# Performance work log

Hardware: AMD Instinct MI355X
Metric: run time of the kernel (lower is better)

Reference implementation:

```python
import jax, jax.numpy as jnp
import numpy as np
from jax import lax

B, N, C = 8, 8192, 64
ODR, K, OUT = 4, 32, 128
S = N // ODR
EPS = 1e-5


def _lbr(h, W, b, g, be):
    # h: [M, K, Cin] -> linear -> BN (training-mode batch stats over (M,K) per channel) -> relu
    y = jnp.einsum('mki,oi->mko', h, W) + b
    mean = y.mean(axis=(0, 1))
    var = ((y - mean) ** 2).mean(axis=(0, 1))  # biased var, as torch BN uses for normalization
    y = (y - mean) * lax.rsqrt(var + EPS) * g + be
    return jax.nn.relu(y)


def setup_inputs() -> dict:
    key = jax.random.key(0)
    ks = jax.random.split(key, 12)
    x = jax.random.normal(ks[0], (B, N, C), dtype=jnp.float32)
    coor = jax.random.normal(ks[1], (B, N, 3), dtype=jnp.float32)
    indx = jax.random.permutation(ks[2], N)[:S]  # like torch.randperm(N)[:S]
    w1 = jax.random.normal(ks[3], (OUT, 2 * C), dtype=jnp.float32) * (2 * C) ** -0.5
    b1 = jax.random.normal(ks[4], (OUT,), dtype=jnp.float32) * 0.01
    g1 = jax.random.uniform(ks[5], (OUT,), dtype=jnp.float32, minval=0.5, maxval=1.5)
    be1 = jax.random.normal(ks[6], (OUT,), dtype=jnp.float32) * 0.01
    w2 = jax.random.normal(ks[7], (OUT, OUT), dtype=jnp.float32) * OUT ** -0.5
    b2 = jax.random.normal(ks[8], (OUT,), dtype=jnp.float32) * 0.01
    g2 = jax.random.uniform(ks[9], (OUT,), dtype=jnp.float32, minval=0.5, maxval=1.5)
    be2 = jax.random.normal(ks[10], (OUT,), dtype=jnp.float32) * 0.01
    return dict(x=x, coor=coor, indx=indx, w1=w1, b1=b1, g1=g1, be1=be1,
                w2=w2, b2=b2, g2=g2, be2=be2)


def reference(x, coor, indx, w1, b1, g1, be1, w2, b2, g2, be2):
    sampled_coor = coor[:, indx, :]  # [B,S,3]
    sampled_x = x[:, indx, :]        # [B,S,C]
    # pairwise squared distances [B,S,N]
    dist = jnp.sum((coor[:, None, :, :] - sampled_coor[:, :, None, :]) ** 2, axis=-1)
    # k smallest distances == argsort(dist)[..., :K]
    _, knn_idx = lax.top_k(-dist, K)  # [B,S,K]
    knn_x = jax.vmap(lambda xb, ib: xb[ib])(x, knn_idx)  # [B,S,K,C]
    rep_x = jnp.broadcast_to(sampled_x[:, :, None, :], (x.shape[0], S, K, x.shape[2]))
    feat = jnp.concatenate([rep_x, knn_x - rep_x], axis=-1)  # [B,S,K,2C]
    feat = feat.reshape(x.shape[0] * S, K, 2 * x.shape[2])
    h = _lbr(feat, w1, b1, g1, be1)
    h = _lbr(h, w2, b2, g2, be2)
    h = h.reshape(x.shape[0], S, K, -1)
    out = jnp.max(h, axis=2)  # [B,S,OUT]
    return out, sampled_coor
```

## Files before the change

### kernel.cpp

```cpp
#include <hip/hip_runtime.h>
#include <stdint.h>


#define N_    8192
#define GPB_  16

typedef __attribute__((ext_vector_type(8))) short bf8;
typedef __attribute__((ext_vector_type(16))) float f32x16;
typedef __attribute__((ext_vector_type(2))) float f32x2;

__device__ __forceinline__ unsigned int bf1u(float f) {
  unsigned int u = __float_as_uint(f);
  return (u + 0x7fffu + ((u >> 16) & 1u)) >> 16;
}
__device__ __forceinline__ unsigned int bfpair(float lo, float hi) {
  return bf1u(lo) | (bf1u(hi) << 16);
}

__device__ __forceinline__ f32x2 pk_add(f32x2 a, f32x2 b) {
  f32x2 d;
  asm("v_pk_add_f32 %0, %1, %2" : "=v"(d) : "v"(a), "v"(b));
  return d;
}
__device__ __forceinline__ f32x2 pk_mul(f32x2 a, f32x2 b) {
  f32x2 d;
  asm("v_pk_mul_f32 %0, %1, %2" : "=v"(d) : "v"(a), "v"(b));
  return d;
}

__global__ __launch_bounds__(256) void kprep(const float* __restrict__ w1,
                                             const float* __restrict__ w2,
                                             const float* __restrict__ coor,
                                             const int* __restrict__ indx,
                                             unsigned short* __restrict__ w1b,
                                             unsigned short* __restrict__ w2b,
                                             float* __restrict__ outc,
                                             float* __restrict__ soa) {
  int e = blockIdx.x * 256 + threadIdx.x;
  if (e < 16384) {
    w1b[e] = (unsigned short)bf1u(w1[e]);
  } else if (e < 32768) {
    int e2 = e - 16384;
    w2b[e2] = (unsigned short)bf1u(w2[e2]);
  } else if (e < 81920) {
    int e2 = e - 32768;
    int bs = e2 / 3, c = e2 - bs * 3;
    int b = bs >> 11, s = bs & 2047;
    outc[e2] = coor[(b * N_ + indx[s]) * 3 + c];
  } else {
    int p = e - 81920;
    const int b = p >> 13, i = p & 8191;
    const float* src = coor + (size_t)p * 3;
    float* dst = soa + b * 24576;
    dst[i]         = src[0];
    dst[8192 + i]  = src[1];
    dst[16384 + i] = src[2];
  }
}

__global__ __launch_bounds__(256, 8) void kknn(const float* __restrict__ soa,
                                               const int* __restrict__ indx,
                                               int* __restrict__ knn) {
  __shared__ __align__(16) float4 sdist4[4 * 256];
  __shared__ float sTw[8];
  __shared__ unsigned long long cands[192];
  __shared__ int ccnt;

  const int gid = blockIdx.x;
  const int b = gid >> 11, s = gid & 2047;
  const int tid = threadIdx.x;
  const int w = tid >> 6, lane = tid & 63;
  const int hl = lane & 31;
  const float* Xb = soa + b * 24576;
  const float* Yb = Xb + 8192;
  const float* Zb = Xb + 16384;
  const int qi = indx[s];
  const float qx = Xb[qi], qy = Yb[qi], qz = Zb[qi];
  const f32x2 nqx = {-qx, -qx}, nqy = {-qy, -qy}, nqz = {-qz, -qz};

  f32x2 rd[8];
  float dmA = 3.4e38f, dmB = 3.4e38f;
#pragma unroll
  for (int it = 0; it < 8; ++it) {
    const int ofs = (it << 10) + (tid << 2);
    union { float4 f4; f32x2 h[2]; } X, Y, Z;
    X.f4 = *(const float4*)(Xb + ofs);
    Y.f4 = *(const float4*)(Yb + ofs);
    Z.f4 = *(const float4*)(Zb + ofs);
    const f32x2 dxl = pk_add(X.h[0], nqx), dyl = pk_add(Y.h[0], nqy),
                dzl = pk_add(Z.h[0], nqz);
    const f32x2 dxh = pk_add(X.h[1], nqx), dyh = pk_add(Y.h[1], nqy),
                dzh = pk_add(Z.h[1], nqz);
    const f32x2 sl =
        pk_add(pk_add(pk_mul(dxl, dxl), pk_mul(dyl, dyl)), pk_mul(dzl, dzl));
    const f32x2 sh =
        pk_add(pk_add(pk_mul(dxh, dxh), pk_mul(dyh, dyh)), pk_mul(dzh, dzh));
    dmA = fminf(fminf(sl.x, sl.y), dmA);
    dmB = fminf(fminf(sh.x, sh.y), dmB);
    if (it < 4) {
      rd[it * 2] = sl;
      rd[it * 2 + 1] = sh;
    } else {
      union { float4 f4; f32x2 h[2]; } st;
      st.h[0] = sl;
      st.h[1] = sh;
      sdist4[((it - 4) << 8) + tid] = st.f4;
    }
  }
  float dmin = fminf(dmA, dmB);
  if (tid == 0) ccnt = 0;
  if (tid < 192) cands[tid] = ~0ULL;

  float v = dmin;
#pragma unroll
  for (int k = 2; k <= 32; k <<= 1) {
#pragma unroll
    for (int j = k >> 1; j >= 1; j >>= 1) {
      const float o = __shfl_xor(v, j, 64);
      const bool dirAsc = ((hl & k) == 0);
      const bool lower = ((hl & j) == 0);
      const float lo = fminf(v, o), hi = fmaxf(v, o);
      v = (dirAsc == lower) ? lo : hi;
    }
  }
  if (hl == 3) sTw[(w << 1) + (lane >> 5)] = v;
  __syncthreads();
  const float T =
      fmaxf(fmaxf(fmaxf(sTw[0], sTw[1]), fmaxf(sTw[2], sTw[3])),
            fmaxf(fmaxf(sTw[4], sTw[5]), fmaxf(sTw[6], sTw[7])));

#pragma unroll
  for (int t = 0; t < 8; ++t) {
    const int p0 = ((t >> 1) << 10) + (tid << 2) + ((t & 1) << 1);
    const float d0 = rd[t].x, d1 = rd[t].y;
    if (d0 <= T) {
      const int pos = atomicAdd(&ccnt, 1);
      if (pos < 192)
        cands[pos] = ((unsigned long long)__float_as_uint(d0) << 32) |
                     (unsigned int)p0;
    }
    if (d1 <= T) {
      const int pos = atomicAdd(&ccnt, 1);
      if (pos < 192)
        cands[pos] = ((unsigned long long)__float_as_uint(d1) << 32) |
                     (unsigned int)(p0 + 1);
    }
  }
#pragma unroll
  for (int it = 4; it < 8; ++it) {
    const float4 d4 = sdist4[((it - 4) << 8) + tid];
    const int p0 = (it << 10) + (tid << 2);
    const float dd[4] = {d4.x, d4.y, d4.z, d4.w};
#pragma unroll
    for (int j = 0; j < 4; ++j) {
      if (dd[j] <= T) {
        const int pos = atomicAdd(&ccnt, 1);
        if (pos < 192)
          cands[pos] = ((unsigned long long)__float_as_uint(dd[j]) << 32) |
                       (unsigned int)(p0 + j);
      }
    }
  }
  __syncthreads();

  const int E = min(ccnt, 192);
  if (tid < E) {
    const unsigned long long key = cands[tid];
    int rank = 0;
    const int Ep = (E + 3) & ~3;
#pragma unroll 4
    for (int j = 0; j < Ep; ++j) rank += (cands[j] < key) ? 1 : 0;
    if (rank < 32) knn[gid * 32 + rank] = (int)(unsigned int)key;
  }
}

template <int PHASE>
__global__ __launch_bounds__(256, 2) void kphase(
    const float* __restrict__ x, const int* __restrict__ indx,
    const int* __restrict__ knn, const float* __restrict__ b1,
    const unsigned short* __restrict__ w1b, const unsigned short* __restrict__ w2b,
    const float* __restrict__ b2, const float* __restrict__ st1,
    float* __restrict__ part, float* __restrict__ mout) {
  __shared__ __align__(16) unsigned short sxb[2][80];
  __shared__ __align__(16) unsigned short dls[2][32 * 68 + 8];
  __shared__ __align__(16) unsigned short h1[PHASE == 2 ? 2 * 32 * 136 : 8];

  const int tid = threadIdx.x;
  const int w = tid >> 6;
  const int lane = tid & 63;
  const int m = lane & 31, q2 = lane >> 5;
  const int col = (w << 5) + m;
  const int r8 = tid >> 3, c8 = (tid & 7) * 8;

  const int bb = blockIdx.x & 7;
  const int jj = blockIdx.x >> 3;
  const float* xb = x + (size_t)bb * (N_ * 64);
  const int gidbase = (bb << 11) + jj * GPB_;
  const int sbase = jj * GPB_;

  bf8 bf1[8];
#pragma unroll
  for (int t = 0; t < 8; ++t)
    bf1[t] = *(const bf8*)&w1b[col * 128 + t * 16 + q2 * 8];
  bf8 bf2[8];
  float s1 = 0.f, t1 = 0.f, b2v = 0.f;
  if constexpr (PHASE == 2) {
#pragma unroll
    for (int t = 0; t < 8; ++t)
      bf2[t] = *(const bf8*)&w2b[col * 128 + t * 16 + q2 * 8];
    s1 = st1[col];
    t1 = st1[128 + col];
    b2v = b2[col];
  }
  (void)w2b; (void)b2; (void)st1; (void)mout;
  const float b1c = b1[col];

  float sum = 0.f, ssq = 0.f;

  float4 ca_c, cc_c, ga_c, gc_c;
  {
    const int idx0 = indx[sbase];
    const int nbr0 = knn[(size_t)gidbase * 32 + r8];
    const float* c0 = xb + (size_t)idx0 * 64;
    ca_c = *(const float4*)(c0 + c8);
    cc_c = *(const float4*)(c0 + c8 + 4);
    const float* g0 = xb + (size_t)nbr0 * 64;
    ga_c = *(const float4*)(g0 + c8);
    gc_c = *(const float4*)(g0 + c8 + 4);
  }
  int idx_nxt = (GPB_ > 1) ? indx[sbase + 1] : 0;
  int nbr_nxt = (GPB_ > 1) ? knn[(size_t)(gidbase + 1) * 32 + r8] : 0;

#pragma unroll 1
  for (int g = 0; g < GPB_; ++g) {
    const int gid = gidbase + g;
    const int p = g & 1;

    float4 ca_n = ca_c, cc_n = cc_c, ga_n = ga_c, gc_n = gc_c;
    if (g + 1 < GPB_) {
      const float* cn = xb + (size_t)idx_nxt * 64;
      ca_n = *(const float4*)(cn + c8);
      cc_n = *(const float4*)(cn + c8 + 4);
      const float* gn = xb + (size_t)nbr_nxt * 64;
      ga_n = *(const float4*)(gn + c8);
      gc_n = *(const float4*)(gn + c8 + 4);
    }
    if (g + 2 < GPB_) {
      nbr_nxt = knn[(size_t)(gid + 2) * 32 + r8];
      idx_nxt = indx[sbase + g + 2];
    }

    {
      uint2 lo, hi;
      lo.x = bfpair(ga_c.x - ca_c.x, ga_c.y - ca_c.y);
      lo.y = bfpair(ga_c.z - ca_c.z, ga_c.w - ca_c.w);
      hi.x = bfpair(gc_c.x - cc_c.x, gc_c.y - cc_c.y);
      hi.y = bfpair(gc_c.z - cc_c.z, gc_c.w - cc_c.w);
      *(uint2*)&dls[p][r8 * 68 + c8] = lo;
      *(uint2*)&dls[p][r8 * 68 + c8 + 4] = hi;
    }
    if (tid < 8) {
      uint2 lo, hi;
      lo.x = bfpair(ca_c.x, ca_c.y);
      lo.y = bfpair(ca_c.z, ca_c.w);
      hi.x = bfpair(cc_c.x, cc_c.y);
      hi.y = bfpair(cc_c.z, cc_c.w);
      *(uint2*)&sxb[p][tid * 8] = lo;
      *(uint2*)&sxb[p][tid * 8 + 4] = hi;
    }
    asm volatile("s_waitcnt lgkmcnt(0)" ::: "memory");
    __builtin_amdgcn_s_barrier();

    bf8 af[8];
#pragma unroll
    for (int t = 0; t < 4; ++t) {
      union { bf8 v; uint2 u[2]; } fa;
      fa.u[0] = *(const uint2*)&sxb[p][t * 16 + q2 * 8];
      fa.u[1] = *(const uint2*)&sxb[p][t * 16 + q2 * 8 + 4];
      af[t] = fa.v;
    }
#pragma unroll
    for (int t = 0; t < 4; ++t) {
      union { bf8 v; uint2 u[2]; } fa;
      fa.u[0] = *(const uint2*)&dls[p][m * 68 + t * 16 + q2 * 8];
      fa.u[1] = *(const uint2*)&dls[p][m * 68 + t * 16 + q2 * 8 + 4];
      af[4 + t] = fa.v;
    }

    f32x16 acc;
#pragma unroll
    for (int r = 0; r < 16; ++r) acc[r] = b1c;
#pragma unroll
    for (int t = 0; t < 8; ++t)
      acc = __builtin_amdgcn_mfma_f32_32x32x16_bf16(af[t], bf1[t], acc, 0, 0, 0);

    if constexpr (PHASE == 1) {
#pragma unroll
      for (int r = 0; r < 16; ++r) {
        const float v = acc[r];
        sum += v;
        ssq = fmaf(v, v, ssq);
      }
    } else {
      const int hp = p * (32 * 136);
#pragma unroll
      for (int r = 0; r < 16; ++r) {
        const float hv = fmaxf(0.f, fmaf(acc[r], s1, t1));
        const int row = (r & 3) + ((r >> 2) << 3) + (q2 << 2);
        h1[hp + row * 136 + col] = (unsigned short)bf1u(hv);
      }
      asm volatile("s_waitcnt lgkmcnt(0)" ::: "memory");
      __builtin_amdgcn_s_barrier();

      f32x16 acc2;
#pragma unroll
      for (int r = 0; r < 16; ++r) acc2[r] = b2v;
#pragma unroll
      for (int t = 0; t < 8; ++t) {
        const bf8 a2 = *(const bf8*)&h1[hp + m * 136 + t * 16 + q2 * 8];
        acc2 = __builtin_amdgcn_mfma_f32_32x32x16_bf16(a2, bf2[t], acc2, 0, 0, 0);
      }

      float mx = -1e30f;
#pragma unroll
      for (int r = 0; r < 16; ++r) {
        const float v = acc2[r];
        sum += v;
        ssq = fmaf(v, v, ssq);
        mx = fmaxf(mx, v);
      }
      mx = fmaxf(mx, __shfl_xor(mx, 32, 64));
      if (lane < 32) mout[(size_t)gid * 128 + col] = mx;
    }

    ca_c = ca_n;
    cc_c = cc_n;
    ga_c = ga_n;
    gc_c = gc_n;
  }

  sum += __shfl_xor(sum, 32, 64);
  ssq += __shfl_xor(ssq, 32, 64);
  if (lane < 32) {
    part[blockIdx.x * 256 + col] = sum;
    part[blockIdx.x * 256 + 128 + col] = ssq;
  }
}

__global__ __launch_bounds__(256) void kred1(const float* __restrict__ part,
                                             double* __restrict__ dbuf) {
  const int blk = blockIdx.x;
  const int c = threadIdx.x;
  const float* p = part + (size_t)blk * 16 * 256 + c;
  double acc = 0.0;
#pragma unroll
  for (int r = 0; r < 16; ++r) acc += (double)p[r * 256];
  dbuf[blk * 256 + c] = acc;
}

__global__ __launch_bounds__(256) void kred2(const double* __restrict__ dbuf,
                                             const float* __restrict__ gam,
                                             const float* __restrict__ bet,
                                             float* __restrict__ st) {
  __shared__ double sS[256];
  const int c = threadIdx.x;
  double acc = 0.0;
#pragma unroll 8
  for (int i = 0; i < 64; ++i) acc += dbuf[i * 256 + c];
  sS[c] = acc;
  __syncthreads();
  if (c < 128) {
    const double Sv = sS[c], SSv = sS[128 + c];
    const double cnt = 524288.0;
    const double mean = Sv / cnt;
    const double var = SSv / cnt - mean * mean;
    const double scale = (double)gam[c] / sqrt(var + 1e-5);
    st[c] = (float)scale;
    st[128 + c] = (float)((double)bet[c] - mean * scale);
  }
}

__global__ __launch_bounds__(256) void kout(const float* __restrict__ m,
                                            const float* __restrict__ st2,
                                            float* __restrict__ out) {
  const int e4 = blockIdx.x * 256 + threadIdx.x;
  const int o0 = (e4 & 31) * 4;
  const float4 v = ((const float4*)m)[e4];
  const float4 sc = *(const float4*)&st2[o0];
  const float4 sh = *(const float4*)&st2[128 + o0];
  float4 r;
  r.x = fmaxf(0.f, fmaf(v.x, sc.x, sh.x));
  r.y = fmaxf(0.f, fmaf(v.y, sc.y, sh.y));
  r.z = fmaxf(0.f, fmaf(v.z, sc.z, sh.z));
  r.w = fmaxf(0.f, fmaf(v.w, sc.w, sh.w));
  ((float4*)out)[e4] = r;
}

extern "C" void kernel_launch(void* const* d_in, const int* in_sizes, int n_in,
                              void* d_out, int out_size, void* d_ws, size_t ws_size,
                              hipStream_t stream) {
  (void)in_sizes; (void)n_in; (void)out_size; (void)ws_size;
  const float* x    = (const float*)d_in[0];
  const float* coor = (const float*)d_in[1];
  const int*   indx = (const int*)d_in[2];
  const float* w1   = (const float*)d_in[3];
  const float* b1   = (const float*)d_in[4];
  const float* g1   = (const float*)d_in[5];
  const float* be1  = (const float*)d_in[6];
  const float* w2   = (const float*)d_in[7];
  const float* b2   = (const float*)d_in[8];
  const float* g2   = (const float*)d_in[9];
  const float* be2  = (const float*)d_in[10];
  float* out = (float*)d_out;

  char* ws = (char*)d_ws;
  int*            knn   = (int*)(ws + 0);
  float*          mbuf  = (float*)(ws + 2097152);
  float*          part1 = (float*)(ws + 10485760);
  float*          soa   = (float*)(ws + 10485760);
  float*          part2 = (float*)(ws + 12582912);
  unsigned short* w1b   = (unsigned short*)(ws + 14680064);
  unsigned short* w2b   = (unsigned short*)(ws + 14712832);
  float*          st1   = (float*)(ws + 14745600);
  float*          st2   = (float*)(ws + 14746624);
  double*         dbuf  = (double*)(ws + 14747648);

  float* outc = out + 2097152;

  kprep<<<576, 256, 0, stream>>>(w1, w2, coor, indx, w1b, w2b, outc, soa);
  kknn<<<16384, 256, 0, stream>>>(soa, indx, knn);
  kphase<1><<<1024, 256, 0, stream>>>(x, indx, knn, b1, w1b, w2b, b2, nullptr,
                                      part1, nullptr);
  kred1<<<64, 256, 0, stream>>>(part1, dbuf);
  kred2<<<1, 256, 0, stream>>>(dbuf, g1, be1, st1);
  kphase<2><<<1024, 256, 0, stream>>>(x, indx, knn, b1, w1b, w2b, b2, st1,
                                      part2, mbuf);
  kred1<<<64, 256, 0, stream>>>(part2, dbuf);
  kred2<<<1, 256, 0, stream>>>(dbuf, g2, be2, st2);
  kout<<<2048, 256, 0, stream>>>(mbuf, st2, out);
}
```

Measured before the change: 248.8 us.

## Process two groups per loop iteration to halve barriers and deepen prefetch

The main loop of the MLP phase kernels now handles two sampled groups per iteration instead of one. LDS staging buffers grow to four slots and the prefetch of gathered x rows is doubled. Fewer barriers per group are intended to cut synchronisation overhead and give more MFMA work between waits to hide gather latency. The cost is higher register use (two sets of prefetched float4 and two accumulators), which may reduce occupancy under the 2-blocks launch bound.

```diff
diff --git a/kernel.cpp b/kernel.cpp
--- a/kernel.cpp
+++ b/kernel.cpp
@@ -181,8 +181,8 @@
     const unsigned short* __restrict__ w1b, const unsigned short* __restrict__ w2b,
     const float* __restrict__ b2, const float* __restrict__ st1,
     float* __restrict__ part, float* __restrict__ mout) {
-  __shared__ __align__(16) unsigned short sxb[2][80];
-  __shared__ __align__(16) unsigned short dls[2][32 * 68 + 8];
+  __shared__ __align__(16) unsigned short sxb[4][80];
+  __shared__ __align__(16) unsigned short dls[4][32 * 68 + 8];
   __shared__ __align__(16) unsigned short h1[PHASE == 2 ? 2 * 32 * 136 : 8];
 
   const int tid = threadIdx.x;
@@ -217,126 +217,163 @@
 
   float sum = 0.f, ssq = 0.f;
 
-  float4 ca_c, cc_c, ga_c, gc_c;
+  float4 caA, ccA, gaA, gcA, caB, ccB, gaB, gcB;
   {
-    const int idx0 = indx[sbase];
-    const int nbr0 = knn[(size_t)gidbase * 32 + r8];
-    const float* c0 = xb + (size_t)idx0 * 64;
-    ca_c = *(const float4*)(c0 + c8);
-    cc_c = *(const float4*)(c0 + c8 + 4);
-    const float* g0 = xb + (size_t)nbr0 * 64;
-    ga_c = *(const float4*)(g0 + c8);
-    gc_c = *(const float4*)(g0 + c8 + 4);
-  }
-  int idx_nxt = (GPB_ > 1) ? indx[sbase + 1] : 0;
-  int nbr_nxt = (GPB_ > 1) ? knn[(size_t)(gidbase + 1) * 32 + r8] : 0;
+    const int idxA = indx[sbase];
+    const int idxB = indx[sbase + 1];
+    const int nbrA = knn[(size_t)gidbase * 32 + r8];
+    const int nbrB = knn[(size_t)(gidbase + 1) * 32 + r8];
+    const float* cA = xb + (size_t)idxA * 64;
+    caA = *(const float4*)(cA + c8);
+    ccA = *(const float4*)(cA + c8 + 4);
+    const float* gA = xb + (size_t)nbrA * 64;
+    gaA = *(const float4*)(gA + c8);
+    gcA = *(const float4*)(gA + c8 + 4);
+    const float* cB = xb + (size_t)idxB * 64;
+    caB = *(const float4*)(cB + c8);
+    ccB = *(const float4*)(cB + c8 + 4);
+    const float* gB = xb + (size_t)nbrB * 64;
+    gaB = *(const float4*)(gB + c8);
+    gcB = *(const float4*)(gB + c8 + 4);
+  }
+  int idxA2 = (GPB_ > 2) ? indx[sbase + 2] : 0;
+  int idxB2 = (GPB_ > 3) ? indx[sbase + 3] : 0;
+  int nbrA2 = (GPB_ > 2) ? knn[(size_t)(gidbase + 2) * 32 + r8] : 0;
+  int nbrB2 = (GPB_ > 3) ? knn[(size_t)(gidbase + 3) * 32 + r8] : 0;
 
 #pragma unroll 1
-  for (int g = 0; g < GPB_; ++g) {
+  for (int g = 0; g < GPB_; g += 2) {
     const int gid = gidbase + g;
-    const int p = g & 1;
-
-    float4 ca_n = ca_c, cc_n = cc_c, ga_n = ga_c, gc_n = gc_c;
-    if (g + 1 < GPB_) {
-      const float* cn = xb + (size_t)idx_nxt * 64;
-      ca_n = *(const float4*)(cn + c8);
-      cc_n = *(const float4*)(cn + c8 + 4);
-      const float* gn = xb + (size_t)nbr_nxt * 64;
-      ga_n = *(const float4*)(gn + c8);
-      gc_n = *(const float4*)(gn + c8 + 4);
-    }
+    const int p0 = g & 3, p1 = (g + 1) & 3;
+
+    float4 caA_n = caA, ccA_n = ccA, gaA_n = gaA, gcA_n = gcA;
+    float4 caB_n = caB, ccB_n = ccB, gaB_n = gaB, gcB_n = gcB;
     if (g + 2 < GPB_) {
-      nbr_nxt = knn[(size_t)(gid + 2) * 32 + r8];
-      idx_nxt = indx[sbase + g + 2];
+      const float* cA = xb + (size_t)idxA2 * 64;
+      caA_n = *(const float4*)(cA + c8);
+      ccA_n = *(const float4*)(cA + c8 + 4);
+      const float* gA = xb + (size_t)nbrA2 * 64;
+      gaA_n = *(const float4*)(gA + c8);
+      gcA_n = *(const float4*)(gA + c8 + 4);
+      const float* cB = xb + (size_t)idxB2 * 64;
+      caB_n = *(const float4*)(cB + c8);
+      ccB_n = *(const float4*)(cB + c8 + 4);
+      const float* gB = xb + (size_t)nbrB2 * 64;
+      gaB_n = *(const float4*)(gB + c8);
+      gcB_n = *(const float4*)(gB + c8 + 4);
+    }
+    if (g + 4 < GPB_) {
+      nbrA2 = knn[(size_t)(gid + 4) * 32 + r8];
+      nbrB2 = knn[(size_t)(gid + 5) * 32 + r8];
+      idxA2 = indx[sbase + g + 4];
+      idxB2 = indx[sbase + g + 5];
     }
 
     {
       uint2 lo, hi;
-      lo.x = bfpair(ga_c.x - ca_c.x, ga_c.y - ca_c.y);
-      lo.y = bfpair(ga_c.z - ca_c.z, ga_c.w - ca_c.w);
-      hi.x = bfpair(gc_c.x - cc_c.x, gc_c.y - cc_c.y);
-      hi.y = bfpair(gc_c.z - cc_c.z, gc_c.w - cc_c.w);
-      *(uint2*)&dls[p][r8 * 68 + c8] = lo;
-      *(uint2*)&dls[p][r8 * 68 + c8 + 4] = hi;
+      lo.x = bfpair(gaA.x - caA.x, gaA.y - caA.y);
+      lo.y = bfpair(gaA.z - caA.z, gaA.w - caA.w);
+      hi.x = bfpair(gcA.x - ccA.x, gcA.y - ccA.y);
+      hi.y = bfpair(gcA.z - ccA.z, gcA.w - ccA.w);
+      *(uint2*)&dls[p0][r8 * 68 + c8] = lo;
+      *(uint2*)&dls[p0][r8 * 68 + c8 + 4] = hi;
+      lo.x = bfpair(gaB.x - caB.x, gaB.y - caB.y);
+      lo.y = bfpair(gaB.z - caB.z, gaB.w - caB.w);
+      hi.x = bfpair(gcB.x - ccB.x, gcB.y - ccB.y);
+      hi.y = bfpair(gcB.z - ccB.z, gcB.w - ccB.w);
+      *(uint2*)&dls[p1][r8 * 68 + c8] = lo;
+      *(uint2*)&dls[p1][r8 * 68 + c8 + 4] = hi;
     }
     if (tid < 8) {
       uint2 lo, hi;
-      lo.x = bfpair(ca_c.x, ca_c.y);
-      lo.y = bfpair(ca_c.z, ca_c.w);
-      hi.x = bfpair(cc_c.x, cc_c.y);
-      hi.y = bfpair(cc_c.z, cc_c.w);
-      *(uint2*)&sxb[p][tid * 8] = lo;
-      *(uint2*)&sxb[p][tid * 8 + 4] = hi;
+      lo.x = bfpair(caA.x, caA.y);
+      lo.y = bfpair(caA.z, caA.w);
+      hi.x = bfpair(ccA.x, ccA.y);
+      hi.y = bfpair(ccA.z, ccA.w);
+      *(uint2*)&sxb[p0][tid * 8] = lo;
+      *(uint2*)&sxb[p0][tid * 8 + 4] = hi;
+      lo.x = bfpair(caB.x, caB.y);
+      lo.y = bfpair(caB.z, caB.w);
+      hi.x = bfpair(ccB.x, ccB.y);
+      hi.y = bfpair(ccB.z, ccB.w);
+      *(uint2*)&sxb[p1][tid * 8] = lo;
+      *(uint2*)&sxb[p1][tid * 8 + 4] = hi;
     }
     asm volatile("s_waitcnt lgkmcnt(0)" ::: "memory");
     __builtin_amdgcn_s_barrier();
 
-    bf8 af[8];
-#pragma unroll
-    for (int t = 0; t < 4; ++t) {
-      union { bf8 v; uint2 u[2]; } fa;
-      fa.u[0] = *(const uint2*)&sxb[p][t * 16 + q2 * 8];
-      fa.u[1] = *(const uint2*)&sxb[p][t * 16 + q2 * 8 + 4];
-      af[t] = fa.v;
-    }
-#pragma unroll
-    for (int t = 0; t < 4; ++t) {
-      union { bf8 v; uint2 u[2]; } fa;
-      fa.u[0] = *(const uint2*)&dls[p][m * 68 + t * 16 + q2 * 8];
-      fa.u[1] = *(const uint2*)&dls[p][m * 68 + t * 16 + q2 * 8 + 4];
-      af[4 + t] = fa.v;
-    }
-
-    f32x16 acc;
-#pragma unroll
-    for (int r = 0; r < 16; ++r) acc[r] = b1c;
-#pragma unroll
-    for (int t = 0; t < 8; ++t)
-      acc = __builtin_amdgcn_mfma_f32_32x32x16_bf16(af[t], bf1[t], acc, 0, 0, 0);
-
-    if constexpr (PHASE == 1) {
-#pragma unroll
-      for (int r = 0; r < 16; ++r) {
-        const float v = acc[r];
-        sum += v;
-        ssq = fmaf(v, v, ssq);
+#pragma unroll
+    for (int mem = 0; mem < 2; ++mem) {
+      const int pb = mem == 0 ? p0 : p1;
+      bf8 af[8];
+#pragma unroll
+      for (int t = 0; t < 4; ++t) {
+        union { bf8 v; uint2 u[2]; } fa;
+        fa.u[0] = *(const uint2*)&sxb[pb][t * 16 + q2 * 8];
+        fa.u[1] = *(const uint2*)&sxb[pb][t * 16 + q2 * 8 + 4];
+        af[t] = fa.v;
       }
-    } else {
-      const int hp = p * (32 * 136);
-#pragma unroll
-      for (int r = 0; r < 16; ++r) {
-        const float hv = fmaxf(0.f, fmaf(acc[r], s1, t1));
-        const int row = (r & 3) + ((r >> 2) << 3) + (q2 << 2);
-        h1[hp + row * 136 + col] = (unsigned short)bf1u(hv);
+#pragma unroll
+      for (int t = 0; t < 4; ++t) {
+        union { bf8 v; uint2 u[2]; } fa;
+        fa.u[0] = *(const uint2*)&dls[pb][m * 68 + t * 16 + q2 * 8];
+        fa.u[1] = *(const uint2*)&dls[pb][m * 68 + t * 16 + q2 * 8 + 4];
+        af[4 + t] = fa.v;
       }
+      f32x16 acc;
+#pragma unroll
+      for (int r = 0; r < 16; ++r) acc[r] = b1c;
+#pragma unroll
+      for (int t = 0; t < 8; ++t)
+        acc = __builtin_amdgcn_mfma_f32_32x32x16_bf16(af[t], bf1[t], acc, 0, 0, 0);
+
+      if constexpr (PHASE == 1) {
+#pragma unroll
+        for (int r = 0; r < 16; ++r) {
+          const float v = acc[r];
+          sum += v;
+          ssq = fmaf(v, v, ssq);
+        }
+      } else {
+        const int hp = mem * (32 * 136);
+#pragma unroll
+        for (int r = 0; r < 16; ++r) {
+          const float hv = fmaxf(0.f, fmaf(acc[r], s1, t1));
+          const int row = (r & 3) + ((r >> 2) << 3) + (q2 << 2);
+          h1[hp + row * 136 + col] = (unsigned short)bf1u(hv);
+        }
+      }
+    }
+
+    if constexpr (PHASE == 2) {
       asm volatile("s_waitcnt lgkmcnt(0)" ::: "memory");
       __builtin_amdgcn_s_barrier();
-
-      f32x16 acc2;
-#pragma unroll
-      for (int r = 0; r < 16; ++r) acc2[r] = b2v;
-#pragma unroll
-      for (int t = 0; t < 8; ++t) {
-        const bf8 a2 = *(const bf8*)&h1[hp + m * 136 + t * 16 + q2 * 8];
-        acc2 = __builtin_amdgcn_mfma_f32_32x32x16_bf16(a2, bf2[t], acc2, 0, 0, 0);
+#pragma unroll
+      for (int mem = 0; mem < 2; ++mem) {
+        const int hp = mem * (32 * 136);
+        f32x16 acc2;
+#pragma unroll
+        for (int r = 0; r < 16; ++r) acc2[r] = b2v;
+#pragma unroll
+        for (int t = 0; t < 8; ++t) {
+          const bf8 a2 = *(const bf8*)&h1[hp + m * 136 + t * 16 + q2 * 8];
+          acc2 = __builtin_amdgcn_mfma_f32_32x32x16_bf16(a2, bf2[t], acc2, 0, 0, 0);
+        }
+        float mx = -1e30f;
+#pragma unroll
+        for (int r = 0; r < 16; ++r) {
+          const float v = acc2[r];
+          sum += v;
+          ssq = fmaf(v, v, ssq);
+          mx = fmaxf(mx, v);
+        }
+        mx = fmaxf(mx, __shfl_xor(mx, 32, 64));
+        if (lane < 32) mout[(size_t)(gid + mem) * 128 + col] = mx;
       }
-
-      float mx = -1e30f;
-#pragma unroll
-      for (int r = 0; r < 16; ++r) {
-        const float v = acc2[r];
-        sum += v;
-        ssq = fmaf(v, v, ssq);
-        mx = fmaxf(mx, v);
-      }
-      mx = fmaxf(mx, __shfl_xor(mx, 32, 64));
-      if (lane < 32) mout[(size_t)gid * 128 + col] = mx;
-    }
-
-    ca_c = ca_n;
-    cc_c = cc_n;
-    ga_c = ga_n;
-    gc_c = gc_n;
+    }
+
+    caA = caA_n; ccA = ccA_n; gaA = gaA_n; gcA = gcA_n;
+    caB = caB_n; ccB = ccB_n; gaB = gaB_n; gcB = gcB_n;
   }
 
   sum += __shfl_xor(sum, 32, 64);
```

After: 243.4 us, median of 3. 1.02x faster.
